# Performance work log

Measured on AMD Instinct MI355X. Metric: run time of the kernel, lower is better.

## Reference

```python
import jax, jax.numpy as jnp
import numpy as np

# dims: B batch, S src len, D input_size, H rnn hidden, E embedding_dim,
# V = output_size + 2 (vocab + Start/End), T = max target len (+2 for Start/End)
B, S, D, H, E, V, T = 128, 512, 256, 512, 256, 1002, 34
END = V - 1  # 'End' token index


def _gru_layer(x, h0, Wih, Whh, bih, bhh):
    """PyTorch-convention GRU layer. x: [B,T,Din], h0: [B,H].
    Wih: [3H,Din], Whh: [3H,H]. Returns (outputs [B,T,H], h_T [B,H])."""
    def step(h, xt):
        gi = xt @ Wih.T + bih            # [B,3H]
        gh = h @ Whh.T + bhh             # [B,3H]
        i_r, i_z, i_n = jnp.split(gi, 3, axis=-1)
        h_r, h_z, h_n = jnp.split(gh, 3, axis=-1)
        r = jax.nn.sigmoid(i_r + h_r)
        z = jax.nn.sigmoid(i_z + h_z)
        n = jnp.tanh(i_n + r * h_n)
        h_new = (1.0 - z) * n + z * h
        return h_new, h_new
    hT, ys = jax.lax.scan(step, h0, jnp.swapaxes(x, 0, 1))
    return jnp.swapaxes(ys, 0, 1), hT


def _gru_stack(x, h0s, layers):
    """h0s: [L,B,H]; layers: list of (Wih,Whh,bih,bhh). Returns (out, h [L,B,H])."""
    hs = []
    y = x
    for l, (Wih, Whh, bih, bhh) in enumerate(layers):
        y, hT = _gru_layer(y, h0s[l], Wih, Whh, bih, bhh)
        hs.append(hT)
    return y, jnp.stack(hs, axis=0)


def setup_inputs() -> dict:
    key = jax.random.key(0)
    ks = jax.random.split(key, 32)
    sc = 0.05
    inp = {}
    inp['source'] = jax.random.normal(ks[0], (B, S, D), dtype=jnp.float32)
    inp['target_ids'] = jax.random.randint(ks[1], (B, T), 0, V)
    inp['lengths'] = jax.random.randint(ks[2], (B,), 2, T + 1)
    inp['emb'] = sc * jax.random.normal(ks[3], (V, E), dtype=jnp.float32)
    # encoder layer 0 (in=D) and layer 1 (in=H)
    inp['enc_Wih0'] = sc * jax.random.normal(ks[4], (3 * H, D), dtype=jnp.float32)
    inp['enc_Whh0'] = sc * jax.random.normal(ks[5], (3 * H, H), dtype=jnp.float32)
    inp['enc_bih0'] = jnp.zeros((3 * H,), jnp.float32)
    inp['enc_bhh0'] = jnp.zeros((3 * H,), jnp.float32)
    inp['enc_Wih1'] = sc * jax.random.normal(ks[6], (3 * H, H), dtype=jnp.float32)
    inp['enc_Whh1'] = sc * jax.random.normal(ks[7], (3 * H, H), dtype=jnp.float32)
    inp['enc_bih1'] = jnp.zeros((3 * H,), jnp.float32)
    inp['enc_bhh1'] = jnp.zeros((3 * H,), jnp.float32)
    # decoder layer 0 (in=E) and layer 1 (in=H)
    inp['dec_Wih0'] = sc * jax.random.normal(ks[8], (3 * H, E), dtype=jnp.float32)
    inp['dec_Whh0'] = sc * jax.random.normal(ks[9], (3 * H, H), dtype=jnp.float32)
    inp['dec_bih0'] = jnp.zeros((3 * H,), jnp.float32)
    inp['dec_bhh0'] = jnp.zeros((3 * H,), jnp.float32)
    inp['dec_Wih1'] = sc * jax.random.normal(ks[10], (3 * H, H), dtype=jnp.float32)
    inp['dec_Whh1'] = sc * jax.random.normal(ks[11], (3 * H, H), dtype=jnp.float32)
    inp['dec_bih1'] = jnp.zeros((3 * H,), jnp.float32)
    inp['dec_bhh1'] = jnp.zeros((3 * H,), jnp.float32)
    # fc: H -> 5H -> 2H -> V
    inp['fc_W1'] = sc * jax.random.normal(ks[12], (5 * H, H), dtype=jnp.float32)
    inp['fc_b1'] = jnp.zeros((5 * H,), jnp.float32)
    inp['fc_W2'] = sc * jax.random.normal(ks[13], (2 * H, 5 * H), dtype=jnp.float32)
    inp['fc_b2'] = jnp.zeros((2 * H,), jnp.float32)
    inp['fc_W3'] = sc * jax.random.normal(ks[14], (V, 2 * H), dtype=jnp.float32)
    inp['fc_b3'] = jnp.zeros((V,), jnp.float32)
    return inp


def reference(source, target_ids, lengths, emb,
              enc_Wih0, enc_Whh0, enc_bih0, enc_bhh0,
              enc_Wih1, enc_Whh1, enc_bih1, enc_bhh1,
              dec_Wih0, dec_Whh0, dec_bih0, dec_bhh0,
              dec_Wih1, dec_Whh1, dec_bih1, dec_bhh1,
              fc_W1, fc_b1, fc_W2, fc_b2, fc_W3, fc_b3):
    Bx = source.shape[0]
    h0 = jnp.zeros((2, Bx, H), source.dtype)
    # encoder: only final hidden state h [L,B,H] is used
    _, h = _gru_stack(source, h0,
                      [(enc_Wih0, enc_Whh0, enc_bih0, enc_bhh0),
                       (enc_Wih1, enc_Whh1, enc_bih1, enc_bhh1)])
    # decoder over embedded (Start + target + End + pad) sequences
    tg = emb[target_ids]                               # [B,T,E]
    out, _ = _gru_stack(tg, h,
                        [(dec_Wih0, dec_Whh0, dec_bih0, dec_bhh0),
                         (dec_Wih1, dec_Whh1, dec_bih1, dec_bhh1)])
    # pad_packed_sequence zeroes timesteps >= length; sum over time
    mask = (jnp.arange(T)[None, :] < lengths[:, None]).astype(out.dtype)  # [B,T]
    pooled = jnp.einsum('bth,bt->bh', out, mask)       # [B,H]
    x = pooled @ fc_W1.T + fc_b1
    x = x @ fc_W2.T + fc_b2
    x = x @ fc_W3.T + fc_b3
    scores = jax.nn.sigmoid(x)                         # [B,V]
    # CrossEntropyLoss against the 'End' index for every row
    logp = jax.nn.log_softmax(scores, axis=-1)
    loss = -jnp.mean(logp[:, END])
    return loss
```

## Files before the change

kernel.cpp:

```cpp
#include <hip/hip_runtime.h>
#include <hip/hip_bf16.h>
#include <math.h>

#define B_ 128
#define S_ 512
#define D_ 256
#define H_ 512
#define E_ 256
#define V_ 1002
#define T_ 34
#define END_ 1001
#define NWG_TOTAL 128
#define BH (B_ * H_)
#define GPITCH 20

typedef __attribute__((ext_vector_type(8))) short short8;
typedef __attribute__((ext_vector_type(4))) float f32x4;
typedef __attribute__((ext_vector_type(4))) int i32x4;
typedef unsigned long long u64;

__device__ __forceinline__ float bf2f(unsigned short u){
  union { unsigned int i; float f; } x; x.i = ((unsigned int)u) << 16; return x.f;
}
__device__ __forceinline__ unsigned short f2bf(float f){
  union { float f; unsigned int i; } x; x.f = f;
  unsigned int r = x.i + 0x7fffu + ((x.i >> 16) & 1u);
  return (unsigned short)(r >> 16);
}
__device__ __forceinline__ float sigm(float x){ return 1.0f / (1.0f + expf(-x)); }

__device__ __forceinline__ void store_coh8(unsigned short* p, u64 v){
  __hip_atomic_store((u64*)p, v, __ATOMIC_RELAXED, __HIP_MEMORY_SCOPE_AGENT);
}

__device__ __forceinline__ i32x4 load_flags16(const unsigned* p){
  i32x4 r;
  asm volatile("global_load_dwordx4 %0, %1, off sc0 sc1\n\ts_waitcnt vmcnt(0)"
               : "=v"(r) : "v"(p) : "memory");
  return r;
}


__global__ void f2bf_kernel(const float* __restrict__ in, unsigned short* __restrict__ out, int n){
  int i = blockIdx.x * blockDim.x + threadIdx.x;
  int stride = gridDim.x * blockDim.x;
  for (; i < n; i += stride) out[i] = f2bf(in[i]);
}

__global__ void embed_kernel(const float* __restrict__ emb, const int* __restrict__ ids,
                             unsigned short* __restrict__ out){
  int i = blockIdx.x * blockDim.x + threadIdx.x;
  if (i >= B_ * T_ * E_) return;
  int bt = i >> 8;
  int e  = i & (E_ - 1);
  out[i] = f2bf(emb[(size_t)ids[bt] * E_ + e]);
}

__global__ void build_wcat(const float* __restrict__ Wih, const float* __restrict__ Whh,
                           unsigned short* __restrict__ Wcat, int Din){
  int K = Din + H_;
  int total = 2048 * K;
  int i = blockIdx.x * blockDim.x + threadIdx.x;
  int stride = gridDim.x * blockDim.x;
  for (; i < total; i += stride){
    int n = i / K, k = i - n * K;
    int g = n >> 9, j = n & 511;
    float v;
    if (g < 2){
      int r = (g << 9) + j;
      v = (k < Din) ? Wih[(size_t)r * Din + k] : Whh[(size_t)r * H_ + (k - Din)];
    } else if (g == 2){
      v = (k < Din) ? Wih[(size_t)(1024 + j) * Din + k] : 0.0f;
    } else {
      v = (k < Din) ? 0.0f : Whh[(size_t)(1024 + j) * H_ + (k - Din)];
    }
    Wcat[i] = f2bf(v);
  }
}

__global__ void build_bias(const float* __restrict__ bih, const float* __restrict__ bhh,
                           float* __restrict__ out){
  int j = blockIdx.x * blockDim.x + threadIdx.x;
  if (j >= 512) return;
  out[j]        = bih[j] + bhh[j];
  out[512 + j]  = bih[512 + j] + bhh[512 + j];
  out[1024 + j] = bih[1024 + j];
  out[1536 + j] = bhh[1024 + j];
}


template<int KT, int XKT>
__device__ __forceinline__ void run_layer(
    float* gbuf,
    const unsigned short* __restrict__ Wc, const float* __restrict__ bias4,
    const unsigned short* __restrict__ Xbase, int x_rs, int x_ts,
    const unsigned short* __restrict__ Hread,
    unsigned short* Hwrite,
    int T, unsigned round0,
    unsigned* own_flags, int slot,
    unsigned* prod_flags, unsigned prod0,
    u64* hprev,
    int jtile, int mh, int wv, int lane)
{
  constexpr int K   = KT * 32;
  constexpr int KTL = KT / 4;
  const int tid  = threadIdx.x;
  const int ln   = lane & 15;
  const int lk8  = (lane >> 4) << 3;
  const int base_m = mh * 64;
  const int q = wv;

  short8 wreg[4][KTL];
  #pragma unroll
  for (int g = 0; g < 4; ++g)
    #pragma unroll
    for (int k = 0; k < KTL; ++k)
      wreg[g][k] = *reinterpret_cast<const short8*>(
          Wc + (size_t)(g * 512 + jtile * 16 + ln) * K + (size_t)(q * KTL + k) * 32 + lk8);

  const int erow  = tid >> 2;
  const int ecol0 = (tid & 3) << 2;
  const int ej    = (jtile << 4) + ecol0;
  const int egr   = base_m + erow;
  f32x4 bR, bZ, bNI, bNH;
  #pragma unroll
  for (int c = 0; c < 4; ++c){
    bR[c]  = bias4[ej + c];
    bZ[c]  = bias4[512 + ej + c];
    bNI[c] = bias4[1024 + ej + c];
    bNH[c] = bias4[1536 + ej + c];
  }

  for (int t = 0; t < T; ++t){
    if (wv == 0){
      const unsigned own_t  = round0 + (unsigned)t;
      const unsigned prod_t = prod0 + (unsigned)t + 1u;
      const unsigned* pofs = own_flags + (lane & 7) * 4;
      const unsigned* ppfs = prod_flags ? (prod_flags + (lane & 7) * 4) : nullptr;
      for (;;){
        i32x4 f = load_flags16(pofs);
        bool ok = (unsigned)f.x >= own_t && (unsigned)f.y >= own_t &&
                  (unsigned)f.z >= own_t && (unsigned)f.w >= own_t;
        if (ppfs){
          i32x4 g = load_flags16(ppfs);
          ok = ok && (unsigned)g.x >= prod_t && (unsigned)g.y >= prod_t &&
                     (unsigned)g.z >= prod_t && (unsigned)g.w >= prod_t;
        }
        if (__all(ok)) break;
        __builtin_amdgcn_s_sleep(1);
      }
    }
    __syncthreads();

    const unsigned short* Xt  = Xbase + (size_t)t * x_ts;
    const unsigned short* Hin = Hread + (size_t)t * BH;

    f32x4 acc[4][4];
    #pragma unroll
    for (int g = 0; g < 4; ++g)
      #pragma unroll
      for (int mt = 0; mt < 4; ++mt) acc[g][mt] = (f32x4){0.f, 0.f, 0.f, 0.f};

    #pragma unroll
    for (int k = 0; k < KTL; ++k){
      const int kt = q * KTL + k;
      short8 a[4];
      if (kt < XKT){
        #pragma unroll
        for (int mt = 0; mt < 4; ++mt)
          a[mt] = *reinterpret_cast<const short8*>(
              Xt + (size_t)(base_m + mt * 16 + ln) * x_rs + kt * 32 + lk8);
      } else {
        #pragma unroll
        for (int mt = 0; mt < 4; ++mt)
          a[mt] = *reinterpret_cast<const short8*>(
              Hin + (size_t)(base_m + mt * 16 + ln) * H_ + (kt - XKT) * 32 + lk8);
      }
      #pragma unroll
      for (int g = 0; g < 4; ++g)
        #pragma unroll
        for (int mt = 0; mt < 4; ++mt)
          acc[g][mt] = __builtin_amdgcn_mfma_f32_16x16x32_bf16(a[mt], wreg[g][k], acc[g][mt], 0, 0, 0);
    }

    #pragma unroll
    for (int g = 0; g < 4; ++g)
      #pragma unroll
      for (int mt = 0; mt < 4; ++mt){
        const int rl = mt * 16 + ((lane >> 4) << 2);
        #pragma unroll
        for (int i = 0; i < 4; ++i)
          gbuf[((q * 4 + g) * 64 + rl + i) * GPITCH + ln] = acc[g][mt][i];
      }
    __syncthreads();

    {
      f32x4 p0 = (f32x4){0.f,0.f,0.f,0.f}, p1 = p0, p2 = p0, p3 = p0;
      #pragma unroll
      for (int qq = 0; qq < 4; ++qq){
        p0 += *reinterpret_cast<const f32x4*>(gbuf + ((qq * 4 + 0) * 64 + erow) * GPITCH + ecol0);
        p1 += *reinterpret_cast<const f32x4*>(gbuf + ((qq * 4 + 1) * 64 + erow) * GPITCH + ecol0);
        p2 += *reinterpret_cast<const f32x4*>(gbuf + ((qq * 4 + 2) * 64 + erow) * GPITCH + ecol0);
        p3 += *reinterpret_cast<const f32x4*>(gbuf + ((qq * 4 + 3) * 64 + erow) * GPITCH + ecol0);
      }
      u64 hv = *hprev;
      u64 hb = 0;
      #pragma unroll
      for (int c = 0; c < 4; ++c){
        float rr = sigm(p0[c] + bR[c]);
        float zz = sigm(p1[c] + bZ[c]);
        float nn = tanhf(p2[c] + bNI[c] + rr * (p3[c] + bNH[c]));
        float hp = bf2f((unsigned short)(hv >> (16 * c)));
        float hn = (1.0f - zz) * nn + zz * hp;
        hb |= ((u64)f2bf(hn)) << (16 * c);
      }
      *hprev = hb;
      store_coh8(Hwrite + (size_t)t * BH + ((size_t)egr << 9) + ej, hb);
    }

    asm volatile("s_waitcnt vmcnt(0)" ::: "memory");
    __syncthreads();
    if (tid == 0)
      __hip_atomic_store(own_flags + slot, round0 + (unsigned)t + 1u,
                         __ATOMIC_RELAXED, __HIP_MEMORY_SCOPE_AGENT);
  }
}

__global__ __launch_bounds__(256, 1)
void rnn_persistent(
    const unsigned short* __restrict__ src, const unsigned short* __restrict__ tg,
    const unsigned short* __restrict__ Wc_e0, const unsigned short* __restrict__ Wc_e1,
    const unsigned short* __restrict__ Wc_d0, const unsigned short* __restrict__ Wc_d1,
    const float* __restrict__ b_e0, const float* __restrict__ b_e1,
    const float* __restrict__ b_d0, const float* __restrict__ b_d1,
    unsigned short* H0, unsigned short* H1,
    unsigned* flags)
{
  __shared__ __align__(16) float gbuf[16 * 64 * GPITCH];
  __builtin_amdgcn_fence(__ATOMIC_ACQUIRE, "agent");
  const int wg = blockIdx.x;
  const int layer = wg >> 6;
  const int gidx = wg & 63;
  const int jtile = gidx & 31, mh = gidx >> 5;
  const int wv = threadIdx.x >> 6, lane = threadIdx.x & 63;
  unsigned* own  = flags + (size_t)((layer << 1) | mh) * 64;
  unsigned* prod = flags + (size_t)mh * 64;
  u64 hprev = 0;
  if (layer == 0){
    run_layer<24, 8>(gbuf, Wc_e0, b_e0, src, S_ * D_, D_,
                     H0, H0 + BH, S_, 0u, own, jtile, nullptr, 0u, &hprev,
                     jtile, mh, wv, lane);
    run_layer<24, 8>(gbuf, Wc_d0, b_d0, tg, T_ * E_, E_,
                     H0 + (size_t)512 * BH, H0 + (size_t)513 * BH, T_, 512u,
                     own, jtile, nullptr, 0u, &hprev,
                     jtile, mh, wv, lane);
  } else {
    run_layer<32, 16>(gbuf, Wc_e1, b_e1, H0 + BH, H_, BH,
                      H1, H1 + BH, S_, 0u, own, jtile, prod, 0u, &hprev,
                      jtile, mh, wv, lane);
    run_layer<32, 16>(gbuf, Wc_d1, b_d1, H0 + (size_t)513 * BH, H_, BH,
                      H1 + (size_t)512 * BH, H1 + (size_t)513 * BH, T_, 512u,
                      own, jtile, prod, 512u, &hprev,
                      jtile, mh, wv, lane);
  }
}

__global__ __launch_bounds__(256)
void gemm_nt(const unsigned short* __restrict__ A, const unsigned short* __restrict__ W,
             const float* __restrict__ bias,
             unsigned short* __restrict__ outB, float* __restrict__ outF,
             int M, int N, int K, int act)
{
  const int w    = threadIdx.x >> 6;
  const int lane = threadIdx.x & 63;
  const int ln   = lane & 15;
  const int lk8  = (lane >> 4) << 3;
  const int row0 = blockIdx.y * 32;
  const int col0 = blockIdx.x * 256 + w * 64;

  f32x4 acc[2][4];
  #pragma unroll
  for (int a = 0; a < 2; a++)
    #pragma unroll
    for (int g = 0; g < 4; g++) acc[a][g] = (f32x4){0.f, 0.f, 0.f, 0.f};

  const unsigned short* arow0 = A + (size_t)(row0 + ln) * K;
  const unsigned short* arow1 = A + (size_t)(row0 + 16 + ln) * K;
  const unsigned short* wrow[4];
  int ncol[4];
  #pragma unroll
  for (int nt = 0; nt < 4; ++nt){
    int n = col0 + nt * 16 + ln;
    ncol[nt] = n;
    int nc = n < N ? n : (N - 1);
    wrow[nt] = W + (size_t)nc * K;
  }

  const int nk = K >> 5;
  for (int kt = 0; kt < nk; ++kt){
    const int k = (kt << 5) + lk8;
    short8 a0 = *reinterpret_cast<const short8*>(arow0 + k);
    short8 a1 = *reinterpret_cast<const short8*>(arow1 + k);
    #pragma unroll
    for (int nt = 0; nt < 4; ++nt){
      short8 bf = *reinterpret_cast<const short8*>(wrow[nt] + k);
      acc[0][nt] = __builtin_amdgcn_mfma_f32_16x16x32_bf16(a0, bf, acc[0][nt], 0, 0, 0);
      acc[1][nt] = __builtin_amdgcn_mfma_f32_16x16x32_bf16(a1, bf, acc[1][nt], 0, 0, 0);
    }
  }

  #pragma unroll
  for (int nt = 0; nt < 4; ++nt){
    const int n = ncol[nt];
    if (n >= N) continue;
    const float bv = bias ? bias[n] : 0.0f;
    #pragma unroll
    for (int mt = 0; mt < 2; ++mt){
      const int rbase = row0 + mt * 16 + ((lane >> 4) << 2);
      #pragma unroll
      for (int reg = 0; reg < 4; ++reg){
        const int row = rbase + reg;
        if (row >= M) continue;
        float v = acc[mt][nt][reg] + bv;
        if (act == 1) v = sigm(v);
        if (outB) outB[(size_t)row * N + n] = f2bf(v);
        if (outF) outF[(size_t)row * N + n] = v;
      }
    }
  }
}


__global__ void pool_kernel(const unsigned short* __restrict__ H1, const int* __restrict__ lengths,
                            unsigned short* __restrict__ pooled){
  int i = blockIdx.x * blockDim.x + threadIdx.x;
  if (i >= B_ * H_) return;
  int b = i >> 9;
  int j = i & (H_ - 1);
  int len = lengths[b]; if (len > T_) len = T_;
  float s = 0.0f;
  for (int t = 0; t < len; ++t)
    s += bf2f(H1[(size_t)(513 + t) * BH + ((size_t)b << 9) + j]);
  pooled[i] = f2bf(s);
}

__global__ void loss_kernel(const float* __restrict__ scores, float* __restrict__ out){
  __shared__ float wsum[4];
  const int w = threadIdx.x >> 6;
  const int lane = threadIdx.x & 63;
  float acc = 0.0f;
  for (int b = w; b < B_; b += 4){
    const float* row = scores + (size_t)b * V_;
    float vals[16];
    float mx = -1e30f;
    #pragma unroll
    for (int i = 0; i < 16; ++i){
      int c = lane + i * 64;
      vals[i] = (c < V_) ? row[c] : -1e30f;
      mx = fmaxf(mx, vals[i]);
    }
    #pragma unroll
    for (int off = 32; off; off >>= 1) mx = fmaxf(mx, __shfl_xor(mx, off));
    float se = 0.0f;
    #pragma unroll
    for (int i = 0; i < 16; ++i){
      int c = lane + i * 64;
      if (c < V_) se += expf(vals[i] - mx);
    }
    #pragma unroll
    for (int off = 32; off; off >>= 1) se += __shfl_xor(se, off);
    float logp = row[END_] - (mx + logf(se));
    acc += logp;
  }
  if (lane == 0) wsum[w] = acc;
  __syncthreads();
  if (threadIdx.x == 0){
    out[0] = -(wsum[0] + wsum[1] + wsum[2] + wsum[3]) / (float)B_;
  }
}


extern "C" void kernel_launch(void* const* d_in, const int* in_sizes, int n_in,
                              void* d_out, int out_size, void* d_ws, size_t ws_size,
                              hipStream_t stream) {
  const float* source   = (const float*)d_in[0];
  const int*   tgt_ids  = (const int*)  d_in[1];
  const int*   lengths  = (const int*)  d_in[2];
  const float* emb      = (const float*)d_in[3];
  const float* eWih0 = (const float*)d_in[4],  *eWhh0 = (const float*)d_in[5];
  const float* ebih0 = (const float*)d_in[6],  *ebhh0 = (const float*)d_in[7];
  const float* eWih1 = (const float*)d_in[8],  *eWhh1 = (const float*)d_in[9];
  const float* ebih1 = (const float*)d_in[10], *ebhh1 = (const float*)d_in[11];
  const float* dWih0 = (const float*)d_in[12], *dWhh0 = (const float*)d_in[13];
  const float* dbih0 = (const float*)d_in[14], *dbhh0 = (const float*)d_in[15];
  const float* dWih1 = (const float*)d_in[16], *dWhh1 = (const float*)d_in[17];
  const float* dbih1 = (const float*)d_in[18], *dbhh1 = (const float*)d_in[19];
  const float* fcW1 = (const float*)d_in[20], *fcb1 = (const float*)d_in[21];
  const float* fcW2 = (const float*)d_in[22], *fcb2 = (const float*)d_in[23];
  const float* fcW3 = (const float*)d_in[24], *fcb3 = (const float*)d_in[25];

  char* p = (char*)d_ws;
  auto alloc = [&](size_t bytes) -> void* {
    void* r = (void*)p;
    p += (bytes + 255) & ~(size_t)255;
    return r;
  };

  unsigned short* src_bf = (unsigned short*)alloc((size_t)B_ * S_ * D_ * 2);
  unsigned short* tg_bf  = (unsigned short*)alloc((size_t)B_ * T_ * E_ * 2);
  unsigned short* H0 = (unsigned short*)alloc((size_t)547 * BH * 2);
  unsigned short* H1 = (unsigned short*)alloc((size_t)547 * BH * 2);
  unsigned short* Wc_e0 = (unsigned short*)alloc((size_t)2048 * 768  * 2);
  unsigned short* Wc_e1 = (unsigned short*)alloc((size_t)2048 * 1024 * 2);
  unsigned short* Wc_d0 = (unsigned short*)alloc((size_t)2048 * 768  * 2);
  unsigned short* Wc_d1 = (unsigned short*)alloc((size_t)2048 * 1024 * 2);
  float* bias_e0 = (float*)alloc(2048 * 4);
  float* bias_e1 = (float*)alloc(2048 * 4);
  float* bias_d0 = (float*)alloc(2048 * 4);
  float* bias_d1 = (float*)alloc(2048 * 4);
  unsigned short* fcW1b = (unsigned short*)alloc((size_t)2560 * 512  * 2);
  unsigned short* fcW2b = (unsigned short*)alloc((size_t)1024 * 2560 * 2);
  unsigned short* fcW3b = (unsigned short*)alloc((size_t)V_ * 1024 * 2);
  unsigned short* pooled = (unsigned short*)alloc((size_t)B_ * H_ * 2);
  unsigned short* x1_bf  = (unsigned short*)alloc((size_t)B_ * 2560 * 2);
  unsigned short* x2_bf  = (unsigned short*)alloc((size_t)B_ * 1024 * 2);
  float* scores = (float*)alloc((size_t)B_ * V_ * 4);
  unsigned* flags = (unsigned*)alloc(4 * 64 * 4);

  f2bf_kernel<<<8192, 256, 0, stream>>>(source, src_bf, B_ * S_ * D_);
  embed_kernel<<<(B_ * T_ * E_ + 255) / 256, 256, 0, stream>>>(emb, tgt_ids, tg_bf);
  build_wcat<<<2048, 256, 0, stream>>>(eWih0, eWhh0, Wc_e0, D_);
  build_wcat<<<2048, 256, 0, stream>>>(eWih1, eWhh1, Wc_e1, H_);
  build_wcat<<<2048, 256, 0, stream>>>(dWih0, dWhh0, Wc_d0, E_);
  build_wcat<<<2048, 256, 0, stream>>>(dWih1, dWhh1, Wc_d1, H_);
  build_bias<<<2, 256, 0, stream>>>(ebih0, ebhh0, bias_e0);
  build_bias<<<2, 256, 0, stream>>>(ebih1, ebhh1, bias_e1);
  build_bias<<<2, 256, 0, stream>>>(dbih0, dbhh0, bias_d0);
  build_bias<<<2, 256, 0, stream>>>(dbih1, dbhh1, bias_d1);
  f2bf_kernel<<<4096, 256, 0, stream>>>(fcW1, fcW1b, 2560 * 512);
  f2bf_kernel<<<4096, 256, 0, stream>>>(fcW2, fcW2b, 1024 * 2560);
  f2bf_kernel<<<4096, 256, 0, stream>>>(fcW3, fcW3b, V_ * 1024);

  hipMemsetAsync(H0, 0, (size_t)BH * 2, stream);
  hipMemsetAsync(H1, 0, (size_t)BH * 2, stream);
  hipMemsetAsync(flags, 0, 4 * 64 * 4, stream);

  rnn_persistent<<<NWG_TOTAL, 256, 0, stream>>>(
      src_bf, tg_bf, Wc_e0, Wc_e1, Wc_d0, Wc_d1,
      bias_e0, bias_e1, bias_d0, bias_d1,
      H0, H1, flags);

  pool_kernel<<<(B_ * H_ + 255) / 256, 256, 0, stream>>>(H1, lengths, pooled);

  {
    dim3 g1((2560 + 255) / 256, B_ / 32);
    gemm_nt<<<g1, 256, 0, stream>>>(pooled, fcW1b, fcb1, x1_bf, (float*)nullptr,
                                    B_, 2560, 512, 0);
    dim3 g2((1024 + 255) / 256, B_ / 32);
    gemm_nt<<<g2, 256, 0, stream>>>(x1_bf, fcW2b, fcb2, x2_bf, (float*)nullptr,
                                    B_, 1024, 2560, 0);
    dim3 g3((V_ + 255) / 256, B_ / 32);
    gemm_nt<<<g3, 256, 0, stream>>>(x2_bf, fcW3b, fcb3, (unsigned short*)nullptr, scores,
                                    B_, V_, 1024, 1);
  }

  loss_kernel<<<1, 256, 0, stream>>>(scores, (float*)d_out);
}
```

Baseline: 4.923 ms.

## Stage recurrent hidden tile in LDS, dual-store h, remap workgroups across XCDs

Each step, the workgroup now loads its 64-row hidden-state tile from L2 into padded LDS once, and the MFMA A-operands read from there instead of doing per-lane strided global loads. New hidden values are written twice, once with a normal store and once with a system-coherent store, so the data reaches both the local cache and the coherent level. The grid is doubled and half the workgroups exit early, so the remaining ones are spread across XCDs by the low bits of the block index, grouping the same (layer, mh) role on one XCD for L2 locality. This adds an LDS staging pass and a barrier per step, plus double store traffic.

Measured after the change: 6.097 ms. +23.9%, slower.

```diff
diff --git a/kernel.cpp b/kernel.cpp
--- a/kernel.cpp
+++ b/kernel.cpp
@@ -10,8 +10,9 @@
 #define V_ 1002
 #define T_ 34
 #define END_ 1001
-#define NWG_TOTAL 128
+#define NWG_LAUNCH 256
 #define BH (B_ * H_)
+#define HROWB 1040
 #define GPITCH 20
 
 typedef __attribute__((ext_vector_type(8))) short short8;
@@ -29,8 +30,9 @@
 }
 __device__ __forceinline__ float sigm(float x){ return 1.0f / (1.0f + expf(-x)); }
 
-__device__ __forceinline__ void store_coh8(unsigned short* p, u64 v){
-  __hip_atomic_store((u64*)p, v, __ATOMIC_RELAXED, __HIP_MEMORY_SCOPE_AGENT);
+__device__ __forceinline__ void store_dual8(unsigned short* p, u64 v){
+  asm volatile("global_store_dwordx2 %0, %1, off"         :: "v"(p), "v"(v) : "memory");
+  asm volatile("global_store_dwordx2 %0, %1, off sc0 sc1" :: "v"(p), "v"(v) : "memory");
 }
 
 __device__ __forceinline__ i32x4 load_flags16(const unsigned* p){
@@ -38,6 +40,21 @@
   asm volatile("global_load_dwordx4 %0, %1, off sc0 sc1\n\ts_waitcnt vmcnt(0)"
                : "=v"(r) : "v"(p) : "memory");
   return r;
+}
+
+__device__ __forceinline__ void stage_tile_l2(const unsigned short* src, char* dst, int tid){
+  i32x4 r[16];
+  #pragma unroll
+  for (int p = 0; p < 16; ++p){
+    const char* sp = (const char*)src + p * 4096 + tid * 16;
+    asm volatile("global_load_dwordx4 %0, %1, off sc0" : "=v"(r[p]) : "v"(sp));
+  }
+  asm volatile("s_waitcnt vmcnt(0)" ::: "memory");
+  #pragma unroll
+  for (int p = 0; p < 16; ++p){
+    const int off = p * 4096 + tid * 16;
+    *reinterpret_cast<i32x4*>(dst + (off >> 10) * HROWB + (off & 1023)) = r[p];
+  }
 }
 
 
@@ -91,7 +108,7 @@
 
 template<int KT, int XKT>
 __device__ __forceinline__ void run_layer(
-    float* gbuf,
+    char* smem,
     const unsigned short* __restrict__ Wc, const float* __restrict__ bias4,
     const unsigned short* __restrict__ Xbase, int x_rs, int x_ts,
     const unsigned short* __restrict__ Hread,
@@ -110,6 +127,9 @@
   const int base_m = mh * 64;
   const int q = wv;
 
+  char*  hA   = smem;
+  float* gbuf = (float*)(smem + 64 * HROWB);
+
   short8 wreg[4][KTL];
   #pragma unroll
   for (int g = 0; g < 4; ++g)
@@ -155,6 +175,9 @@
     const unsigned short* Xt  = Xbase + (size_t)t * x_ts;
     const unsigned short* Hin = Hread + (size_t)t * BH;
 
+    stage_tile_l2(Hin + ((size_t)base_m << 9), hA, tid);
+    __syncthreads();
+
     f32x4 acc[4][4];
     #pragma unroll
     for (int g = 0; g < 4; ++g)
@@ -174,7 +197,7 @@
         #pragma unroll
         for (int mt = 0; mt < 4; ++mt)
           a[mt] = *reinterpret_cast<const short8*>(
-              Hin + (size_t)(base_m + mt * 16 + ln) * H_ + (kt - XKT) * 32 + lk8);
+              hA + (mt * 16 + ln) * HROWB + ((kt - XKT) * 32 + lk8) * 2);
       }
       #pragma unroll
       for (int g = 0; g < 4; ++g)
@@ -215,7 +238,7 @@
         hb |= ((u64)f2bf(hn)) << (16 * c);
       }
       *hprev = hb;
-      store_coh8(Hwrite + (size_t)t * BH + ((size_t)egr << 9) + ej, hb);
+      store_dual8(Hwrite + (size_t)t * BH + ((size_t)egr << 9) + ej, hb);
     }
 
     asm volatile("s_waitcnt vmcnt(0)" ::: "memory");
@@ -236,29 +259,31 @@
     unsigned short* H0, unsigned short* H1,
     unsigned* flags)
 {
-  __shared__ __align__(16) float gbuf[16 * 64 * GPITCH];
+  __shared__ __align__(16) char smem[64 * HROWB + 16 * 64 * GPITCH * 4];
+  const int wg = blockIdx.x;
+  const int hint = wg & 7;
+  if (hint >= 4) return;
   __builtin_amdgcn_fence(__ATOMIC_ACQUIRE, "agent");
-  const int wg = blockIdx.x;
-  const int layer = wg >> 6;
-  const int gidx = wg & 63;
-  const int jtile = gidx & 31, mh = gidx >> 5;
+  const int layer = hint >> 1;
+  const int mh    = hint & 1;
+  const int jtile = wg >> 3;
   const int wv = threadIdx.x >> 6, lane = threadIdx.x & 63;
   unsigned* own  = flags + (size_t)((layer << 1) | mh) * 64;
   unsigned* prod = flags + (size_t)mh * 64;
   u64 hprev = 0;
   if (layer == 0){
-    run_layer<24, 8>(gbuf, Wc_e0, b_e0, src, S_ * D_, D_,
+    run_layer<24, 8>(smem, Wc_e0, b_e0, src, S_ * D_, D_,
                      H0, H0 + BH, S_, 0u, own, jtile, nullptr, 0u, &hprev,
                      jtile, mh, wv, lane);
-    run_layer<24, 8>(gbuf, Wc_d0, b_d0, tg, T_ * E_, E_,
+    run_layer<24, 8>(smem, Wc_d0, b_d0, tg, T_ * E_, E_,
                      H0 + (size_t)512 * BH, H0 + (size_t)513 * BH, T_, 512u,
                      own, jtile, nullptr, 0u, &hprev,
                      jtile, mh, wv, lane);
   } else {
-    run_layer<32, 16>(gbuf, Wc_e1, b_e1, H0 + BH, H_, BH,
+    run_layer<32, 16>(smem, Wc_e1, b_e1, H0 + BH, H_, BH,
                       H1, H1 + BH, S_, 0u, own, jtile, prod, 0u, &hprev,
                       jtile, mh, wv, lane);
-    run_layer<32, 16>(gbuf, Wc_d1, b_d1, H0 + (size_t)513 * BH, H_, BH,
+    run_layer<32, 16>(smem, Wc_d1, b_d1, H0 + (size_t)513 * BH, H_, BH,
                       H1 + (size_t)512 * BH, H1 + (size_t)513 * BH, T_, 512u,
                       own, jtile, prod, 512u, &hprev,
                       jtile, mh, wv, lane);
@@ -445,7 +470,7 @@
   hipMemsetAsync(H1, 0, (size_t)BH * 2, stream);
   hipMemsetAsync(flags, 0, 4 * 64 * 4, stream);
 
-  rnn_persistent<<<NWG_TOTAL, 256, 0, stream>>>(
+  rnn_persistent<<<NWG_LAUNCH, 256, 0, stream>>>(
       src_bf, tg_bf, Wc_e0, Wc_e1, Wc_d0, Wc_d1,
       bias_e0, bias_e1, bias_d0, bias_d1,
       H0, H1, flags);
```
